# Performance work log

Hardware: AMD Instinct MI355X
Metric: run time of the kernel (lower is better)

The kernel has to match this reference:

```python
import jax, jax.numpy as jnp
import numpy as np

N_ITER = 3

def setup_inputs() -> dict:
    key = jax.random.key(0)
    k1, k2 = jax.random.split(key)
    x = jax.random.normal(k1, (8, 1024, 512), dtype=jnp.float32)
    W = jax.random.normal(k2, (4, 512, 512), dtype=jnp.float32)
    return {"x": x, "W": W}

def reference(x, W):
    # x: [B, N, D], W: [H, D, D]
    B, N, D = x.shape
    H = W.shape[0]
    scale = D ** (-0.5)
    logits = jnp.zeros((B, H, N, N), dtype=x.dtype)
    rw = None
    for _ in range(N_ITER):
        rw = jax.nn.softmax(logits, axis=-1)              # [B, H, N, N]
        # per-head bilinear scores: (x @ W_h) @ x^T * scale, batched over heads
        logits = jnp.einsum('bnd,hde,bme->bhnm', x, W, x) * scale
    # routing_weights @ x, then mean over heads -> [B, N, D]
    out = jnp.einsum('bhnm,bmd->bhnd', rw, x)
    return jnp.mean(out, axis=1)
```

## Files before the change

kernel.cpp:

```cpp
#include <hip/hip_runtime.h>
#include <math.h>

#define B_ 8
#define N_ 1024
#define D_ 512
#define H_ 4
#define ND (N_ * D_)
#define DD (D_ * D_)
#define NN (N_ * N_)

typedef _Float16 f16;
typedef f16 f16x8 __attribute__((ext_vector_type(8)));
typedef float f32x4 __attribute__((ext_vector_type(4)));

typedef __attribute__((address_space(3))) void lds_void;
typedef __attribute__((address_space(1))) void g_void;


#define MFMA16(QR, QC, AV, BV)                                                \
    _Pragma("unroll")                                                         \
    for (int i_ = 0; i_ < 4; ++i_)                                            \
        _Pragma("unroll")                                                     \
        for (int j_ = 0; j_ < 2; ++j_) {                                      \
            acc[(QR)*4+i_][(QC)*2+j_] = __builtin_amdgcn_mfma_f32_16x16x32_f16(AV[i_][0], BV[j_][0], acc[(QR)*4+i_][(QC)*2+j_], 0, 0, 0); \
            acc[(QR)*4+i_][(QC)*2+j_] = __builtin_amdgcn_mfma_f32_16x16x32_f16(AV[i_][1], BV[j_][1], acc[(QR)*4+i_][(QC)*2+j_], 0, 0, 0); \
        }

#define READ_A(AV, PA, HALF)                                                  \
    _Pragma("unroll")                                                         \
    for (int i_ = 0; i_ < 4; ++i_) {                                          \
        const int ra_ = (HALF) * 128 + wr * 64 + i_ * 16 + fr;                \
        AV[i_][0] = *(const f16x8*)(PA + ra_ * 64 + sw0 * 8);                 \
        AV[i_][1] = *(const f16x8*)(PA + ra_ * 64 + sw1 * 8);                 \
    }

#define READ_B(BV, PB, HALF)                                                  \
    _Pragma("unroll")                                                         \
    for (int j_ = 0; j_ < 2; ++j_) {                                          \
        const int rb_ = (HALF) * 128 + wc * 32 + j_ * 16 + fr;                \
        BV[j_][0] = *(const f16x8*)(PB + rb_ * 64 + sw0 * 8);                 \
        BV[j_][1] = *(const f16x8*)(PB + rb_ * 64 + sw1 * 8);                 \
    }

#define PHASE_SYNC_MFMA(QR, QC, AV, BV, STAGE, TAIL)                          \
    __builtin_amdgcn_sched_barrier(0);                                        \
    STAGE;                                                                    \
    __builtin_amdgcn_s_barrier();                                             \
    asm volatile("s_waitcnt lgkmcnt(0)" ::: "memory");                        \
    __builtin_amdgcn_sched_barrier(0);                                        \
    __builtin_amdgcn_s_setprio(1);                                            \
    MFMA16(QR, QC, AV, BV);                                                   \
    __builtin_amdgcn_s_setprio(0);                                            \
    TAIL;                                                                     \
    __builtin_amdgcn_s_barrier();

template<int LDA, int LDB, int LDC, int KTOT>
__device__ __forceinline__ void gemm256(
    const f16* __restrict__ A, const f16* __restrict__ B,
    f16* __restrict__ C, float scale, int m0, int n0)
{
    constexpr int NT = KTOT / 64;
    __shared__ f16 sA0[256 * 64];
    __shared__ f16 sB0[256 * 64];
    __shared__ f16 sA1[256 * 64];
    __shared__ f16 sB1[256 * 64];

    const int t = threadIdx.x;
    const int w = t >> 6, l = t & 63;
    const int fr = l & 15, fq = l >> 4;
    const int wr = w >> 2, wc = w & 3;
    const int lr = l >> 3, lc = l & 7;
    const int swc = lc ^ lr;
    const int sw0 = fq ^ (fr & 7);
    const int sw1 = (4 + fq) ^ (fr & 7);

    f32x4 acc[8][4] = {};

    auto stageA = [&](f16* buf, int half, int kt) {
#pragma unroll
        for (int i = 0; i < 2; ++i) {
            const int r0 = half * 128 + i * 64 + w * 8;
            const f16* g = A + (size_t)(m0 + r0 + lr) * LDA + kt * 64 + swc * 8;
            __builtin_amdgcn_global_load_lds((g_void*)g, (lds_void*)(buf + r0 * 64), 16, 0, 0);
        }
    };
    auto stageB = [&](f16* buf, int half, int kt) {
#pragma unroll
        for (int i = 0; i < 2; ++i) {
            const int r0 = half * 128 + i * 64 + w * 8;
            const f16* g = B + (size_t)(n0 + r0 + lr) * LDB + kt * 64 + swc * 8;
            __builtin_amdgcn_global_load_lds((g_void*)g, (lds_void*)(buf + r0 * 64), 16, 0, 0);
        }
    };

    stageA(sA0, 0, 0); stageB(sB0, 0, 0);
    stageA(sA0, 1, 0); stageB(sB0, 1, 0);
    if (NT > 1) { stageA(sA1, 0, 1); stageB(sB1, 0, 1); }
    asm volatile("s_waitcnt vmcnt(4)" ::: "memory");
    __builtin_amdgcn_s_barrier();

#pragma unroll
    for (int kt = 0; kt < NT; ++kt) {
        f16* cA = (kt & 1) ? sA1 : sA0;
        f16* cB = (kt & 1) ? sB1 : sB0;
        f16* nA = (kt & 1) ? sA0 : sA1;
        f16* nB = (kt & 1) ? sB0 : sB1;

        f16x8 av0[4][2], av1[4][2], bv0[2][2], bv1[2][2];

        READ_A(av0, cA, 0);
        READ_B(bv0, cB, 0);
        PHASE_SYNC_MFMA(0, 0, av0, bv0,
            { if (kt + 1 < NT) stageA(nA, 1, kt + 1); }, {});

        READ_B(bv1, cB, 1);
        PHASE_SYNC_MFMA(0, 1, av0, bv1,
            { if (kt + 1 < NT) stageB(nB, 1, kt + 1); }, {});

        READ_A(av1, cA, 1);
        PHASE_SYNC_MFMA(1, 1, av1, bv1,
            { if (kt + 2 < NT) stageA(cA, 0, kt + 2); }, {});

        PHASE_SYNC_MFMA(1, 0, av1, bv0,
            { if (kt + 2 < NT) stageB(cB, 0, kt + 2); },
            { if (kt + 2 < NT) { asm volatile("s_waitcnt vmcnt(4)" ::: "memory"); }
              else             { asm volatile("s_waitcnt vmcnt(0)" ::: "memory"); } });
    }

#pragma unroll
    for (int ri = 0; ri < 8; ++ri)
#pragma unroll
        for (int cj = 0; cj < 4; ++cj)
#pragma unroll
            for (int rr = 0; rr < 4; ++rr) {
                const int row = m0 + (ri >> 2) * 128 + wr * 64 + (ri & 3) * 16 + fq * 4 + rr;
                const int col = n0 + (cj >> 1) * 128 + wc * 32 + (cj & 1) * 16 + fr;
                C[(size_t)row * LDC + col] = (f16)(acc[ri][cj][rr] * scale);
            }
}

template<int LDA, int LDB, int LDC, int KTOT>
__device__ __forceinline__ void single_core_f32(
    const f16* __restrict__ A, const f16* __restrict__ B0,
    float* __restrict__ C, int n0, int c0)
{
    __shared__ f16 sA[128 * 32];
    __shared__ f16 sB0[128 * 32];

    const int t = threadIdx.x;
    const int w = t >> 6;
    const int l = t & 63;
    const int lrow = l >> 2;
    const int lch  = l & 3;
    const int wr = w >> 1, wc = w & 1;
    const int fr = l & 15;
    const int fq = l >> 4;

    f32x4 acc[4][4] = {};

    for (int k0 = 0; k0 < KTOT; k0 += 32) {
#pragma unroll
        for (int i = 0; i < 2; ++i) {
            const int rb  = w * 2 + i;
            const int row = rb * 16 + lrow;
            const f16* ga = A + (size_t)(n0 + row) * LDA + k0 + lch * 8;
            __builtin_amdgcn_global_load_lds((g_void*)ga, (lds_void*)(sA + rb * 512), 16, 0, 0);
            const f16* gb0 = B0 + (size_t)(c0 + row) * LDB + k0 + lch * 8;
            __builtin_amdgcn_global_load_lds((g_void*)gb0, (lds_void*)(sB0 + rb * 512), 16, 0, 0);
        }
        __syncthreads();

        f16x8 a[4], b0[4];
#pragma unroll
        for (int i = 0; i < 4; ++i) {
            a[i]  = *(const f16x8*)(sA  + (wr * 64 + i * 16 + fr) * 32 + fq * 8);
            b0[i] = *(const f16x8*)(sB0 + (wc * 64 + i * 16 + fr) * 32 + fq * 8);
        }

#pragma unroll
        for (int i = 0; i < 4; ++i)
#pragma unroll
            for (int j = 0; j < 4; ++j)
                acc[i][j] = __builtin_amdgcn_mfma_f32_16x16x32_f16(a[i], b0[j], acc[i][j], 0, 0, 0);
        __syncthreads();
    }

#pragma unroll
    for (int i = 0; i < 4; ++i)
#pragma unroll
        for (int j = 0; j < 4; ++j)
#pragma unroll
            for (int r = 0; r < 4; ++r) {
                const int row = n0 + wr * 64 + i * 16 + fq * 4 + r;
                const int col = c0 + wc * 64 + j * 16 + fr;
                C[(size_t)row * LDC + col] = acc[i][j][r];
            }
}

__global__ __launch_bounds__(512, 2) void k_g1(
    const f16* __restrict__ xfh, const f16* __restrict__ wTh,
    f16* __restrict__ Yh)
{
    const int i = blockIdx.x;
    const int b = i & 7;
    const int li = i >> 3;
    const int h = li >> 3;
    const int tile = li & 7;
    const int m0 = (tile >> 1) * 256;
    const int n0 = (tile & 1) * 256;
    const int z = b * 4 + h;
    gemm256<D_, D_, D_, D_>(
        xfh + (size_t)b * ND,
        wTh + (size_t)h * DD,
        Yh + (size_t)z * ND, 1.0f, m0, n0);
}

__global__ __launch_bounds__(512, 2) void k_g2(
    const f16* __restrict__ Yh, const f16* __restrict__ xfh,
    f16* __restrict__ S)
{
    const int i = blockIdx.x;
    const int b = i & 7;
    const int li = i >> 3;
    const int h = li >> 4;
    const int tile = li & 15;
    const int m0 = (tile >> 2) * 256;
    const int n0 = (tile & 3) * 256;
    const int z = b * 4 + h;
    gemm256<D_, D_, N_, D_>(
        Yh + (size_t)z * ND,
        xfh + (size_t)b * ND,
        S + (size_t)z * NN, 0.044194173824159216f, m0, n0);
}

__global__ __launch_bounds__(256) void softmax_mean(
    const f16* __restrict__ S, f16* __restrict__ Pb)
{
    const int wave = threadIdx.x >> 6;
    const int l = threadIdx.x & 63;
    const int i = blockIdx.x;
    const int b = i & 7;
    const int rg = i >> 3;
    const int row = rg * 4 + wave;

    float o[16];
#pragma unroll
    for (int k = 0; k < 16; ++k) o[k] = 0.f;

#pragma unroll
    for (int h = 0; h < 4; ++h) {
        const f16x8* p = (const f16x8*)(S + ((size_t)(b * 4 + h) * N_ + row) * N_);
        f16x8 v0 = p[l * 2], v1 = p[l * 2 + 1];
        float f[16];
#pragma unroll
        for (int k = 0; k < 8; ++k) { f[k] = (float)v0[k]; f[k + 8] = (float)v1[k]; }
        float m = f[0];
#pragma unroll
        for (int k = 1; k < 16; ++k) m = fmaxf(m, f[k]);
#pragma unroll
        for (int off = 32; off > 0; off >>= 1) m = fmaxf(m, __shfl_xor(m, off));
        float s = 0.f;
#pragma unroll
        for (int k = 0; k < 16; ++k) { f[k] = __expf(f[k] - m); s += f[k]; }
#pragma unroll
        for (int off = 32; off > 0; off >>= 1) s += __shfl_xor(s, off);
        const float q = 0.25f / s;
#pragma unroll
        for (int k = 0; k < 16; ++k) o[k] += f[k] * q;
    }

    f16x8 o0, o1;
#pragma unroll
    for (int k = 0; k < 8; ++k) { o0[k] = (f16)o[k]; o1[k] = (f16)o[k + 8]; }
    f16x8* qp = (f16x8*)(Pb + ((size_t)b * N_ + row) * N_);
    qp[l * 2] = o0;
    qp[l * 2 + 1] = o1;
}

__global__ __launch_bounds__(256, 2) void k_g4b(
    const f16* __restrict__ Pb, const f16* __restrict__ xT,
    float* __restrict__ out)
{
    const int i = blockIdx.x;
    const int b = i & 7;
    const int li = i >> 3;
    const int m0 = (li >> 2) * 128;
    const int d0 = (li & 3) * 128;
    single_core_f32<N_, N_, D_, N_>(
        Pb + (size_t)b * NN,
        xT + (size_t)b * ND,
        out + (size_t)b * ND, m0, d0);
}

__global__ __launch_bounds__(256) void decomp_xw(
    const float* __restrict__ x, const float* __restrict__ W,
    f16* __restrict__ xfh, f16* __restrict__ xT, f16* __restrict__ wTh)
{
    __shared__ f16 tile[64][65];
    __shared__ float tw[64][65];
    const int t = threadIdx.x;
    const int z = blockIdx.z;
    if (z < 8) {
        const int b = z, n0 = blockIdx.y * 64, d0 = blockIdx.x * 64;
        const float* xb = x + (size_t)b * ND;
#pragma unroll
        for (int p = 0; p < 16; ++p) {
            const int idx = t + p * 256;
            const int r = idx >> 6, c = idx & 63;
            const float v = xb[(size_t)(n0 + r) * D_ + d0 + c];
            const f16 h = (f16)v;
            xfh[(size_t)b * ND + (size_t)(n0 + r) * D_ + d0 + c] = h;
            tile[r][c] = h;
        }
        __syncthreads();
#pragma unroll
        for (int p = 0; p < 16; ++p) {
            const int idx = t + p * 256;
            const int r = idx >> 6, c = idx & 63;
            xT[(size_t)b * ND + (size_t)(d0 + r) * N_ + n0 + c] = tile[c][r];
        }
    } else {
        if (blockIdx.y >= 8) return;
        const int h = z - 8, d0 = blockIdx.y * 64, e0 = blockIdx.x * 64;
        const float* Wh = W + (size_t)h * DD;
#pragma unroll
        for (int p = 0; p < 16; ++p) {
            const int idx = t + p * 256;
            const int r = idx >> 6, c = idx & 63;
            tw[r][c] = Wh[(size_t)(d0 + r) * D_ + e0 + c];
        }
        __syncthreads();
#pragma unroll
        for (int p = 0; p < 16; ++p) {
            const int idx = t + p * 256;
            const int r = idx >> 6, c = idx & 63;
            wTh[(size_t)h * DD + (size_t)(e0 + r) * D_ + d0 + c] = (f16)tw[c][r];
        }
    }
}

extern "C" void kernel_launch(void* const* d_in, const int* in_sizes, int n_in,
                              void* d_out, int out_size, void* d_ws, size_t ws_size,
                              hipStream_t stream) {
    const float* x = (const float*)d_in[0];
    const float* W = (const float*)d_in[1];
    float* out = (float*)d_out;

    char* ws = (char*)d_ws;
    const size_t MB = 1024 * 1024;
    f16*   xfh = (f16*)(ws + 0 * MB);
    f16*   xT  = (f16*)(ws + 8 * MB);
    f16*   wTh = (f16*)(ws + 16 * MB);
    f16*   Yh  = (f16*)(ws + 20 * MB);
    f16*   S   = (f16*)(ws + 52 * MB);
    f16*   Pb  = (f16*)(ws + 116 * MB);

    decomp_xw<<<dim3(8, 16, 12), 256, 0, stream>>>(x, W, xfh, xT, wTh);

    k_g1<<<dim3(256), 512, 0, stream>>>(xfh, wTh, Yh);
    k_g2<<<dim3(512), 512, 0, stream>>>(Yh, xfh, S);
    softmax_mean<<<dim3(2048), 256, 0, stream>>>(S, Pb);
    k_g4b<<<dim3(256), 256, 0, stream>>>(Pb, xT, out);
}
```

Before: 171.3 us.

## Overlap LDS fragment reads with MFMA by splitting each phase into halves

Restructures the gemm256 main loop to process two k-tiles per iteration with register-renamed fragment buffers. Each phase now issues half of its MFMAs, then the LDS reads for the next phase and the global-to-LDS staging, then the remaining MFMAs, so LDS latency hides behind matrix work. One barrier per phase is removed. It requires an even tile count, and the reordered reads/stages rely on barrier placement being correct to avoid LDS hazards.

```diff
diff --git a/kernel.cpp b/kernel.cpp
--- a/kernel.cpp
+++ b/kernel.cpp
@@ -17,14 +17,16 @@
 typedef __attribute__((address_space(1))) void g_void;
 
 
-#define MFMA16(QR, QC, AV, BV)                                                \
+#define MFMA8(QR, QC, AV, BV, IB)                                             \
     _Pragma("unroll")                                                         \
-    for (int i_ = 0; i_ < 4; ++i_)                                            \
+    for (int i_ = 0; i_ < 2; ++i_) {                                          \
+        const int ii_ = (IB) + i_;                                            \
         _Pragma("unroll")                                                     \
         for (int j_ = 0; j_ < 2; ++j_) {                                      \
-            acc[(QR)*4+i_][(QC)*2+j_] = __builtin_amdgcn_mfma_f32_16x16x32_f16(AV[i_][0], BV[j_][0], acc[(QR)*4+i_][(QC)*2+j_], 0, 0, 0); \
-            acc[(QR)*4+i_][(QC)*2+j_] = __builtin_amdgcn_mfma_f32_16x16x32_f16(AV[i_][1], BV[j_][1], acc[(QR)*4+i_][(QC)*2+j_], 0, 0, 0); \
-        }
+            acc[(QR)*4+ii_][(QC)*2+j_] = __builtin_amdgcn_mfma_f32_16x16x32_f16(AV[ii_][0], BV[j_][0], acc[(QR)*4+ii_][(QC)*2+j_], 0, 0, 0); \
+            acc[(QR)*4+ii_][(QC)*2+j_] = __builtin_amdgcn_mfma_f32_16x16x32_f16(AV[ii_][1], BV[j_][1], acc[(QR)*4+ii_][(QC)*2+j_], 0, 0, 0); \
+        }                                                                     \
+    }
 
 #define READ_A(AV, PA, HALF)                                                  \
     _Pragma("unroll")                                                         \
@@ -42,17 +44,21 @@
         BV[j_][1] = *(const f16x8*)(PB + rb_ * 64 + sw1 * 8);                 \
     }
 
-#define PHASE_SYNC_MFMA(QR, QC, AV, BV, STAGE, TAIL)                          \
-    __builtin_amdgcn_sched_barrier(0);                                        \
-    STAGE;                                                                    \
+#define PHASE_RA(QR, QC, AV, BV, READS, STAGE, TAIL)                          \
     __builtin_amdgcn_s_barrier();                                             \
     asm volatile("s_waitcnt lgkmcnt(0)" ::: "memory");                        \
     __builtin_amdgcn_sched_barrier(0);                                        \
     __builtin_amdgcn_s_setprio(1);                                            \
-    MFMA16(QR, QC, AV, BV);                                                   \
+    MFMA8(QR, QC, AV, BV, 0);                                                 \
     __builtin_amdgcn_s_setprio(0);                                            \
-    TAIL;                                                                     \
-    __builtin_amdgcn_s_barrier();
+    __builtin_amdgcn_sched_barrier(0);                                        \
+    READS;                                                                    \
+    __builtin_amdgcn_sched_barrier(0);                                        \
+    STAGE;                                                                    \
+    __builtin_amdgcn_s_setprio(1);                                            \
+    MFMA8(QR, QC, AV, BV, 2);                                                 \
+    __builtin_amdgcn_s_setprio(0);                                            \
+    TAIL;
 
 template<int LDA, int LDB, int LDC, int KTOT>
 __device__ __forceinline__ void gemm256(
@@ -60,6 +66,7 @@
     f16* __restrict__ C, float scale, int m0, int n0)
 {
     constexpr int NT = KTOT / 64;
+    static_assert(NT >= 2 && (NT % 2) == 0, "NT must be even");
     __shared__ f16 sA0[256 * 64];
     __shared__ f16 sB0[256 * 64];
     __shared__ f16 sA1[256 * 64];
@@ -95,37 +102,41 @@
 
     stageA(sA0, 0, 0); stageB(sB0, 0, 0);
     stageA(sA0, 1, 0); stageB(sB0, 1, 0);
-    if (NT > 1) { stageA(sA1, 0, 1); stageB(sB1, 0, 1); }
+    stageA(sA1, 0, 1); stageB(sB1, 0, 1);
     asm volatile("s_waitcnt vmcnt(4)" ::: "memory");
     __builtin_amdgcn_s_barrier();
 
-#pragma unroll
-    for (int kt = 0; kt < NT; ++kt) {
-        f16* cA = (kt & 1) ? sA1 : sA0;
-        f16* cB = (kt & 1) ? sB1 : sB0;
-        f16* nA = (kt & 1) ? sA0 : sA1;
-        f16* nB = (kt & 1) ? sB0 : sB1;
-
-        f16x8 av0[4][2], av1[4][2], bv0[2][2], bv1[2][2];
-
-        READ_A(av0, cA, 0);
-        READ_B(bv0, cB, 0);
-        PHASE_SYNC_MFMA(0, 0, av0, bv0,
-            { if (kt + 1 < NT) stageA(nA, 1, kt + 1); }, {});
-
-        READ_B(bv1, cB, 1);
-        PHASE_SYNC_MFMA(0, 1, av0, bv1,
-            { if (kt + 1 < NT) stageB(nB, 1, kt + 1); }, {});
-
-        READ_A(av1, cA, 1);
-        PHASE_SYNC_MFMA(1, 1, av1, bv1,
-            { if (kt + 2 < NT) stageA(cA, 0, kt + 2); }, {});
-
-        PHASE_SYNC_MFMA(1, 0, av1, bv0,
-            { if (kt + 2 < NT) stageB(cB, 0, kt + 2); },
-            { if (kt + 2 < NT) { asm volatile("s_waitcnt vmcnt(4)" ::: "memory"); }
-              else             { asm volatile("s_waitcnt vmcnt(0)" ::: "memory"); } });
-    }
+    f16x8 X[4][2], Y[4][2], U[2][2], V[2][2];
+    READ_A(X, sA0, 0);
+    READ_B(U, sB0, 0);
+
+#define TAILCNT(KT)                                                           \
+    { if ((KT) + 2 < NT) { asm volatile("s_waitcnt vmcnt(4)" ::: "memory"); } \
+      else               { asm volatile("s_waitcnt vmcnt(0)" ::: "memory"); } }
+
+#pragma unroll
+    for (int tt = 0; tt < NT / 2; ++tt) {
+        const int te = 2 * tt, to = 2 * tt + 1;
+        PHASE_RA(0, 0, X, U, { READ_B(V, sB0, 1); },
+                 { if (te + 1 < NT) stageA(sA1, 1, te + 1); }, {});
+        PHASE_RA(0, 1, X, V, { READ_A(Y, sA0, 1); },
+                 { if (te + 1 < NT) stageB(sB1, 1, te + 1); }, {});
+        PHASE_RA(1, 1, Y, V, {},
+                 { if (te + 2 < NT) stageA(sA0, 0, te + 2); }, {});
+        PHASE_RA(1, 0, Y, U,
+                 { if (te + 1 < NT) { READ_A(X, sA1, 0); READ_B(V, sB1, 0); } },
+                 { if (te + 2 < NT) stageB(sB0, 0, te + 2); }, TAILCNT(te));
+        PHASE_RA(0, 0, X, V, { READ_B(U, sB1, 1); },
+                 { if (to + 1 < NT) stageA(sA0, 1, to + 1); }, {});
+        PHASE_RA(0, 1, X, U, { READ_A(Y, sA1, 1); },
+                 { if (to + 1 < NT) stageB(sB0, 1, to + 1); }, {});
+        PHASE_RA(1, 1, Y, U, {},
+                 { if (to + 2 < NT) stageA(sA1, 0, to + 2); }, {});
+        PHASE_RA(1, 0, Y, V,
+                 { if (to + 1 < NT) { READ_A(X, sA0, 0); READ_B(U, sB0, 0); } },
+                 { if (to + 2 < NT) stageB(sB1, 0, to + 2); }, TAILCNT(to));
+    }
+#undef TAILCNT
 
 #pragma unroll
     for (int ri = 0; ri < 8; ++ri)
```

New measurement: 169.6 us. About the same (-1.0%).
